# Kernel optimization log

Hardware: AMD Instinct MI355X
Metric: run time of the kernel (lower is better)

The kernel has to match this reference:

```python
import jax, jax.numpy as jnp
import numpy as np
import math

B, N, D, H, F = 2, 2048, 512, 8, 2048
DH = D // H
LN_EPS = 1e-5
PHASE_ALPHA = 0.1


def _layernorm(x, g, b):
    mu = jnp.mean(x, axis=-1, keepdims=True)
    var = jnp.mean(jnp.square(x - mu), axis=-1, keepdims=True)
    return (x - mu) * jax.lax.rsqrt(var + LN_EPS) * g + b


def setup_inputs() -> dict:
    key = jax.random.key(0)
    ks = jax.random.split(key, 16)
    s = 0.02
    return {
        "h": jax.random.normal(ks[0], (B, N, D), dtype=jnp.float32),
        "phases": jax.random.normal(ks[1], (B, N, H), dtype=jnp.float32),
        "mask": jnp.zeros((B, N), dtype=bool),
        "Wq": jax.random.normal(ks[2], (D, D), dtype=jnp.float32) * s,
        "Wk": jax.random.normal(ks[3], (D, D), dtype=jnp.float32) * s,
        "Wp": jax.random.normal(ks[4], (D, H), dtype=jnp.float32) * s,
        "bp": jnp.zeros((H,), dtype=jnp.float32),
        "Wv": jax.random.normal(ks[5], (D, D), dtype=jnp.float32) * s,
        "Wo": jax.random.normal(ks[6], (D, D), dtype=jnp.float32) * s,
        "W1": jax.random.normal(ks[7], (D, F), dtype=jnp.float32) * s,
        "b1": jnp.zeros((F,), dtype=jnp.float32),
        "W2": jax.random.normal(ks[8], (F, D), dtype=jnp.float32) * s,
        "b2": jnp.zeros((D,), dtype=jnp.float32),
        "g1": jnp.ones((D,), dtype=jnp.float32),
        "be1": jnp.zeros((D,), dtype=jnp.float32),
        "g2": jnp.ones((D,), dtype=jnp.float32),
        "be2": jnp.zeros((D,), dtype=jnp.float32),
        "Wph": jax.random.normal(ks[9], (D, H), dtype=jnp.float32) * s,
        "bph": jnp.zeros((H,), dtype=jnp.float32),
    }


def reference(h, phases, mask, Wq, Wk, Wp, bp, Wv, Wo, W1, b1, W2, b2, g1, be1, g2, be2, Wph, bph):
    # --- HarmonicEdgeLayer ---
    Q = (h @ Wq).reshape(B, N, H, DH)  # (B,N,H,dh)
    K = (h @ Wk).reshape(B, N, H, DH)
    scores = jnp.einsum("bnhd,bmhd->bhnm", Q, K) / math.sqrt(DH)  # (B,H,N,N)
    ph = h @ Wp + bp                       # (B,N,H)
    phi = jnp.transpose(ph, (0, 2, 1))     # (B,H,N)
    harmonic = jnp.cos(phi[:, :, :, None] - phi[:, :, None, :])  # (B,H,N,N)
    scores = scores * (1.0 + harmonic) * 0.5
    scores = jnp.where(mask[:, None, None, :], -jnp.inf, scores)
    edge_weights = jax.nn.softmax(scores, axis=-1)  # (B,H,N,N)

    # --- HarmonicNodeUpdate ---
    V = (h @ Wv).reshape(B, N, H, DH)
    messages = jnp.einsum("bhnm,bmhd->bnhd", edge_weights, V).reshape(B, N, D)
    messages = messages @ Wo
    h1 = _layernorm(h + messages, g1, be1)
    ffn = jax.nn.gelu(h1 @ W1 + b1, approximate=False) @ W2 + b2
    h2 = _layernorm(h1 + ffn, g2, be2)

    # --- PhaseUpdate ---
    phases_new = phases + PHASE_ALPHA * jnp.tanh(h2 @ Wph + bph) * math.pi

    # convergence metric
    delta = jnp.mean(jnp.linalg.norm(h2 - h, axis=-1))
    return h2, phases_new, delta
```

## Files before the change

kernel.cpp:

```cpp
#include <hip/hip_runtime.h>
#include <math.h>

#define BB 2
#define NN 2048
#define DD 512
#define HH 8
#define DHH 64
#define FF 2048
#define MROWS (BB*NN)
#define LN_EPS 1e-5f
#define PHASE_ALPHA 0.1f
#define PI_F 3.14159265358979323846f
#define SCALE 0.125f
#define QLD (3*DD)
#define LOG2E 1.44269504088896340736f

typedef __attribute__((ext_vector_type(8))) short  bf16x8;
typedef __attribute__((ext_vector_type(4))) float  f32x4;
typedef __attribute__((ext_vector_type(4))) unsigned short us4;

__device__ __forceinline__ unsigned short f2bf(float x) {
    unsigned int u = __float_as_uint(x);
    u += 0x7fffu + ((u >> 16) & 1u);
    return (unsigned short)(u >> 16);
}

#if __has_builtin(__builtin_amdgcn_exp2f)
#define EXP2(x) __builtin_amdgcn_exp2f(x)
#else
#define EXP2(x) exp2f(x)
#endif

__device__ __forceinline__ unsigned pk_bf16(float a, float b) {
    unsigned r;
    asm("v_cvt_pk_bf16_f32 %0, %1, %2" : "=v"(r) : "v"(a), "v"(b));
    return r;
}

__global__ __launch_bounds__(256) void convert_bf16_kernel(
    const float* __restrict__ X, unsigned short* __restrict__ Y, int n8)
{
    int i = blockIdx.x*256 + threadIdx.x;
    if (i >= n8) return;
    const float4 a = *(const float4*)&X[i*8];
    const float4 b = *(const float4*)&X[i*8 + 4];
    uint4 o;
    o.x = (unsigned)f2bf(a.x) | ((unsigned)f2bf(a.y) << 16);
    o.y = (unsigned)f2bf(a.z) | ((unsigned)f2bf(a.w) << 16);
    o.z = (unsigned)f2bf(b.x) | ((unsigned)f2bf(b.y) << 16);
    o.w = (unsigned)f2bf(b.z) | ((unsigned)f2bf(b.w) << 16);
    *(uint4*)&Y[i*8] = o;
}

__global__ __launch_bounds__(256) void wtrans_kernel(
    const float* __restrict__ W, unsigned short* __restrict__ WT, int K, int N)
{
    __shared__ unsigned short T[32][33];
    const int k0 = blockIdx.y*32, n0 = blockIdx.x*32;
    const int r = threadIdx.x >> 3, cc = (threadIdx.x & 7)*4;
    float4 v = *(const float4*)&W[(size_t)(k0 + r)*N + n0 + cc];
    T[cc+0][r] = f2bf(v.x); T[cc+1][r] = f2bf(v.y);
    T[cc+2][r] = f2bf(v.z); T[cc+3][r] = f2bf(v.w);
    __syncthreads();
    us4 o; o.x = T[r][cc]; o.y = T[r][cc+1]; o.z = T[r][cc+2]; o.w = T[r][cc+3];
    *(us4*)&WT[(size_t)(n0 + r)*K + k0 + cc] = o;
}

__global__ __launch_bounds__(256) void vtrans_kernel(
    const unsigned short* __restrict__ qkv, unsigned short* __restrict__ VT)
{
    __shared__ unsigned short T[32][33];
    const int b = blockIdx.z;
    const int n0 = blockIdx.x*32, c0 = blockIdx.y*32;
    const int r = threadIdx.x >> 3, cc = (threadIdx.x & 7)*4;
    us4 v = *(const us4*)&qkv[((size_t)b*NN + n0 + r)*QLD + 2*DD + c0 + cc];
    T[cc+0][r] = v.x; T[cc+1][r] = v.y; T[cc+2][r] = v.z; T[cc+3][r] = v.w;
    __syncthreads();
    const int cg = c0 + r;
    const int hh = cg >> 6, dh = cg & 63;
    us4 o; o.x = T[r][cc]; o.y = T[r][cc+1]; o.z = T[r][cc+2]; o.w = T[r][cc+3];
    *(us4*)&VT[(((size_t)b*HH + hh)*DHH + dh)*NN + n0 + cc] = o;
}

template<int BM, int BN, int SPLITK, int OUTBF16, int BIAS, int ACT, int ATOMIC>
__global__ __launch_bounds__(256, 2) void mfma_gemm(
    const unsigned short* __restrict__ A, const unsigned short* __restrict__ BT,
    const float* __restrict__ bias, void* __restrict__ Cout,
    int M, int Nc, int K)
{
    constexpr int FM = BM/32, FN = BN/32;
    constexpr int ROWS = BM + BN;
    constexpr int NLOAD = ROWS*8/256;
    __shared__ unsigned short Ss[ROWS][72];

    const int tid = threadIdx.x;
    const int w = tid >> 6, lane = tid & 63;
    const int c = lane & 15, g = lane >> 4;
    const int wr = w >> 1, wc = w & 1;
    const int bm = blockIdx.y*BM, bn = blockIdx.x*BN;
    const int k0 = (SPLITK > 1) ? blockIdx.z * (K / SPLITK) : 0;
    const int NT = (K / SPLITK) / 64;

    f32x4 zero = {0.f, 0.f, 0.f, 0.f};
    f32x4 acc[FM][FN];
    #pragma unroll
    for (int i = 0; i < FM; ++i)
        #pragma unroll
        for (int j = 0; j < FN; ++j) acc[i][j] = zero;

    uint4 pf[NLOAD];
    #pragma unroll
    for (int l = 0; l < NLOAD; ++l) {
        const int i = tid + l*256;
        const int r = i >> 3, kc = (i & 7)*8;
        const unsigned short* src = (r < BM) ? &A [(size_t)(bm + r)*K + k0 + kc]
                                             : &BT[(size_t)(bn + r - BM)*K + k0 + kc];
        pf[l] = *(const uint4*)src;
    }

    for (int kt = 0; kt < NT; ++kt) {
        __syncthreads();
        #pragma unroll
        for (int l = 0; l < NLOAD; ++l) {
            const int i = tid + l*256;
            *(uint4*)&Ss[i >> 3][(i & 7)*8] = pf[l];
        }
        __syncthreads();
        if (kt + 1 < NT) {
            #pragma unroll
            for (int l = 0; l < NLOAD; ++l) {
                const int i = tid + l*256;
                const int r = i >> 3, kc = (i & 7)*8;
                const unsigned short* src = (r < BM)
                    ? &A [(size_t)(bm + r)*K + k0 + (kt+1)*64 + kc]
                    : &BT[(size_t)(bn + r - BM)*K + k0 + (kt+1)*64 + kc];
                pf[l] = *(const uint4*)src;
            }
        }
        #pragma unroll
        for (int ks = 0; ks < 2; ++ks) {
            bf16x8 af[FM], bfr[FN];
            #pragma unroll
            for (int mf = 0; mf < FM; ++mf)
                af[mf] = *(const bf16x8*)&Ss[wr*(BM/2) + mf*16 + c][ks*32 + g*8];
            #pragma unroll
            for (int nf = 0; nf < FN; ++nf)
                bfr[nf] = *(const bf16x8*)&Ss[BM + wc*(BN/2) + nf*16 + c][ks*32 + g*8];
            #pragma unroll
            for (int mf = 0; mf < FM; ++mf)
                #pragma unroll
                for (int nf = 0; nf < FN; ++nf)
                    acc[mf][nf] = __builtin_amdgcn_mfma_f32_16x16x32_bf16(
                        af[mf], bfr[nf], acc[mf][nf], 0, 0, 0);
        }
    }

    #pragma unroll
    for (int mf = 0; mf < FM; ++mf)
        #pragma unroll
        for (int nf = 0; nf < FN; ++nf) {
            const int col = bn + wc*(BN/2) + nf*16 + c;
            const float bv = BIAS ? bias[col] : 0.f;
            #pragma unroll
            for (int r = 0; r < 4; ++r) {
                const int row = bm + wr*(BM/2) + mf*16 + g*4 + r;
                float x = acc[mf][nf][r] + bv;
                if (ACT == 1) x = 0.5f * x * (1.f + erff(x * 0.70710678118654752f));
                if (ATOMIC)       atomicAdd(&((float*)Cout)[(size_t)row*Nc + col], x);
                else if (OUTBF16) ((unsigned short*)Cout)[(size_t)row*Nc + col] = f2bf(x);
                else              ((float*)Cout)[(size_t)row*Nc + col] = x;
            }
        }
}

__global__ __launch_bounds__(256) void phase_proj_kernel(
    const float* __restrict__ X, const float* __restrict__ Wp,
    const float* __restrict__ bp, float* __restrict__ cosPt, float* __restrict__ sinPt)
{
    __shared__ float Wl[DD*HH];
    for (int i = threadIdx.x; i < DD*HH; i += 256) Wl[i] = Wp[i];
    __syncthreads();
    int row = blockIdx.x*32 + (threadIdx.x >> 3);
    int hh  = threadIdx.x & 7;
    const float* xr = X + (size_t)row * DD;
    float acc = bp[hh];
    for (int k = 0; k < DD; k += 4) {
        float4 xv = *(const float4*)&xr[k];
        acc += xv.x*Wl[(k  )*HH+hh] + xv.y*Wl[(k+1)*HH+hh]
             + xv.z*Wl[(k+2)*HH+hh] + xv.w*Wl[(k+3)*HH+hh];
    }
    const int b = row >> 11, n = row & (NN-1);
    cosPt[((size_t)b*HH + hh)*NN + n] = cosf(acc);
    sinPt[((size_t)b*HH + hh)*NN + n] = sinf(acc);
}

__global__ __launch_bounds__(256) void phase_update_kernel(
    const float* __restrict__ H2, const float* __restrict__ Wph,
    const float* __restrict__ bph, const float* __restrict__ phases,
    float* __restrict__ phases_out)
{
    __shared__ float Wl[DD*HH];
    for (int i = threadIdx.x; i < DD*HH; i += 256) Wl[i] = Wph[i];
    __syncthreads();
    int row = blockIdx.x*32 + (threadIdx.x >> 3);
    int hh  = threadIdx.x & 7;
    const float* xr = H2 + (size_t)row * DD;
    float acc = bph[hh];
    for (int k = 0; k < DD; k += 4) {
        float4 xv = *(const float4*)&xr[k];
        acc += xv.x*Wl[(k  )*HH+hh] + xv.y*Wl[(k+1)*HH+hh]
             + xv.z*Wl[(k+2)*HH+hh] + xv.w*Wl[(k+3)*HH+hh];
    }
    phases_out[row*HH + hh] = phases[row*HH + hh] + PHASE_ALPHA * tanhf(acc) * PI_F;
}

__global__ __launch_bounds__(256, 4) void attn_kernel(
    const unsigned short* __restrict__ qkv, const unsigned short* __restrict__ VT,
    const float* __restrict__ cosPt, const float* __restrict__ sinPt,
    const unsigned char* __restrict__ mask, unsigned short* __restrict__ msgb)
{
    __shared__ float Os[64][36];
    __shared__ float MwS[4][32], LwS[4][32];
    __shared__ unsigned short Pl[4][32][40];

    const int tid = threadIdx.x;
    const int w = tid >> 6, lane = tid & 63;
    const int c = lane & 15, g = lane >> 4;
    const int qBase = blockIdx.x * 32;
    const int hh = blockIdx.y, b = blockIdx.z;
    const size_t rowOff = (size_t)b * NN;
    const int bh = b*HH + hh;
    const size_t cosBase = (size_t)bh * NN;
    const float A = 0.5f * SCALE * LOG2E;

    for (int i = tid; i < 64*36; i += 256) ((float*)Os)[i] = 0.f;

    bf16x8 qf[2][2];
    #pragma unroll
    for (int nf = 0; nf < 2; ++nf)
        #pragma unroll
        for (int ks = 0; ks < 2; ++ks)
            qf[nf][ks] = *(const bf16x8*)&qkv[(rowOff + qBase + nf*16 + c)*QLD
                                              + hh*DHH + ks*32 + g*8];
    float cqs[2], sqs[2];
    #pragma unroll
    for (int nf = 0; nf < 2; ++nf) {
        cqs[nf] = A * cosPt[cosBase + qBase + nf*16 + c];
        sqs[nf] = A * sinPt[cosBase + qBase + nf*16 + c];
    }

    f32x4 zero = {0.f, 0.f, 0.f, 0.f};
    f32x4 acc[4][2];
    #pragma unroll
    for (int i = 0; i < 4; ++i)
        #pragma unroll
        for (int j = 0; j < 2; ++j) acc[i][j] = zero;
    float mst[2] = {-INFINITY, -INFINITY}, lst[2] = {0.f, 0.f};

    __syncthreads();

    for (int s = w; s < NN/32; s += 4) {
        const int kb0 = s * 32;
        f32x4 st[2][2];
        #pragma unroll
        for (int mf = 0; mf < 2; ++mf) {
            bf16x8 kf0 = *(const bf16x8*)&qkv[(rowOff + kb0 + mf*16 + c)*QLD + DD + hh*DHH + g*8];
            bf16x8 kf1 = *(const bf16x8*)&qkv[(rowOff + kb0 + mf*16 + c)*QLD + DD + hh*DHH + 32 + g*8];
            #pragma unroll
            for (int nf = 0; nf < 2; ++nf) {
                st[mf][nf] = __builtin_amdgcn_mfma_f32_16x16x32_bf16(kf0, qf[nf][0], zero, 0, 0, 0);
                st[mf][nf] = __builtin_amdgcn_mfma_f32_16x16x32_bf16(kf1, qf[nf][1], st[mf][nf], 0, 0, 0);
            }
        }
        #pragma unroll
        for (int mf = 0; mf < 2; ++mf) {
            const int keyb = kb0 + mf*16 + g*4;
            const f32x4 ck = *(const f32x4*)&cosPt[cosBase + keyb];
            const f32x4 sk = *(const f32x4*)&sinPt[cosBase + keyb];
            const unsigned int mk = *(const unsigned int*)&mask[rowOff + keyb];
            f32x4 mbias;
            #pragma unroll
            for (int r = 0; r < 4; ++r)
                mbias[r] = ((mk >> (8*r)) & 0xff) ? -INFINITY : 0.f;
            #pragma unroll
            for (int nf = 0; nf < 2; ++nf)
                #pragma unroll
                for (int r = 0; r < 4; ++r) {
                    const float factor = fmaf(cqs[nf], ck[r], fmaf(sqs[nf], sk[r], A));
                    st[mf][nf][r] = fmaf(st[mf][nf][r], factor, mbias[r]);
                }
        }
        #pragma unroll
        for (int nf = 0; nf < 2; ++nf) {
            float tmax = fmaxf(fmaxf(st[0][nf][0], st[0][nf][1]), fmaxf(st[0][nf][2], st[0][nf][3]));
            tmax = fmaxf(tmax, fmaxf(fmaxf(st[1][nf][0], st[1][nf][1]), fmaxf(st[1][nf][2], st[1][nf][3])));
            tmax = fmaxf(tmax, __shfl_xor(tmax, 16));
            tmax = fmaxf(tmax, __shfl_xor(tmax, 32));
            if (!__all(tmax <= mst[nf])) {
                const float mnew = fmaxf(mst[nf], tmax);
                const float corr = (mst[nf] == -INFINITY) ? 0.f : EXP2(mst[nf] - mnew);
                lst[nf] *= corr;
                #pragma unroll
                for (int mo = 0; mo < 4; ++mo)
                    #pragma unroll
                    for (int r = 0; r < 4; ++r) acc[mo][nf][r] *= corr;
                mst[nf] = mnew;
            }
            const float mcur = mst[nf];
            float psum = 0.f;
            unsigned short* prow = &Pl[w][nf*16 + c][0];
            #pragma unroll
            for (int mf = 0; mf < 2; ++mf) {
                float p0 = EXP2(st[mf][nf][0] - mcur);
                float p1 = EXP2(st[mf][nf][1] - mcur);
                float p2 = EXP2(st[mf][nf][2] - mcur);
                float p3 = EXP2(st[mf][nf][3] - mcur);
                psum += (p0 + p1) + (p2 + p3);
                uint2 pk; pk.x = pk_bf16(p0, p1); pk.y = pk_bf16(p2, p3);
                *(uint2*)&prow[mf*16 + g*4] = pk;
            }
            psum += __shfl_xor(psum, 16);
            psum += __shfl_xor(psum, 32);
            lst[nf] += psum;
        }
        bf16x8 vf[4], pfr[2];
        #pragma unroll
        for (int mo = 0; mo < 4; ++mo)
            vf[mo] = *(const bf16x8*)&VT[((size_t)bh*DHH + mo*16 + c)*NN + kb0 + g*8];
        #pragma unroll
        for (int nf = 0; nf < 2; ++nf)
            pfr[nf] = *(const bf16x8*)&Pl[w][nf*16 + c][g*8];
        #pragma unroll
        for (int mo = 0; mo < 4; ++mo)
            #pragma unroll
            for (int nf = 0; nf < 2; ++nf)
                acc[mo][nf] = __builtin_amdgcn_mfma_f32_16x16x32_bf16(
                    vf[mo], pfr[nf], acc[mo][nf], 0, 0, 0);
    }

    if (lane < 16) {
        #pragma unroll
        for (int nf = 0; nf < 2; ++nf) {
            MwS[w][nf*16 + lane] = mst[nf];
            LwS[w][nf*16 + lane] = lst[nf];
        }
    }
    __syncthreads();
    float fac[2];
    #pragma unroll
    for (int nf = 0; nf < 2; ++nf) {
        const int q = nf*16 + c;
        float M = fmaxf(fmaxf(MwS[0][q], MwS[1][q]), fmaxf(MwS[2][q], MwS[3][q]));
        float L = LwS[0][q]*EXP2(MwS[0][q]-M) + LwS[1][q]*EXP2(MwS[1][q]-M)
                + LwS[2][q]*EXP2(MwS[2][q]-M) + LwS[3][q]*EXP2(MwS[3][q]-M);
        fac[nf] = EXP2(mst[nf] - M) / L;
    }
    #pragma unroll
    for (int mo = 0; mo < 4; ++mo)
        #pragma unroll
        for (int nf = 0; nf < 2; ++nf)
            #pragma unroll
            for (int r = 0; r < 4; ++r)
                atomicAdd(&Os[mo*16 + g*4 + r][nf*16 + c], acc[mo][nf][r] * fac[nf]);
    __syncthreads();

    const int q = tid >> 3, dh0 = (tid & 7) * 8;
    unsigned int ov[4];
    #pragma unroll
    for (int i = 0; i < 4; ++i)
        ov[i] = (unsigned)f2bf(Os[dh0 + 2*i][q]) | ((unsigned)f2bf(Os[dh0 + 2*i + 1][q]) << 16);
    unsigned short* op = &msgb[(rowOff + qBase + q)*DD + hh*DHH + dh0];
    *(uint4*)&op[0] = *(uint4*)&ov[0];
}

template<int WITH_DELTA, int WBF16, int YBIAS>
__global__ __launch_bounds__(256) void ln_kernel(
    const float* __restrict__ x, const float* __restrict__ y,
    const float* __restrict__ g, const float* __restrict__ bvec,
    const float* __restrict__ ybias,
    float* __restrict__ out, unsigned short* __restrict__ outb,
    const float* __restrict__ href, float* __restrict__ deltaAcc)
{
    const int row = blockIdx.x;
    const int tid = threadIdx.x;
    const size_t base = (size_t)row * DD + tid*2;
    float2 xv = *(const float2*)(x + base);
    float2 yv = *(const float2*)(y + base);
    float v0 = xv.x + yv.x;
    float v1 = xv.y + yv.y;
    if (YBIAS) { v0 += ybias[tid*2]; v1 += ybias[tid*2+1]; }
    float s  = v0 + v1;
    float sq = v0*v0 + v1*v1;
    #pragma unroll
    for (int m = 1; m < 64; m <<= 1) {
        s  += __shfl_xor(s,  m, 64);
        sq += __shfl_xor(sq, m, 64);
    }
    __shared__ float redS[4], redQ[4];
    int wv = tid >> 6;
    if ((tid & 63) == 0) { redS[wv] = s; redQ[wv] = sq; }
    __syncthreads();
    s  = redS[0] + redS[1] + redS[2] + redS[3];
    sq = redQ[0] + redQ[1] + redQ[2] + redQ[3];
    float mu  = s * (1.f/DD);
    float var = sq * (1.f/DD) - mu*mu;
    float inv = rsqrtf(var + LN_EPS);
    float o0 = (v0 - mu)*inv*g[tid*2  ] + bvec[tid*2  ];
    float o1 = (v1 - mu)*inv*g[tid*2+1] + bvec[tid*2+1];
    float2 ov; ov.x = o0; ov.y = o1;
    *(float2*)(out + base) = ov;
    if (WBF16)
        ((unsigned int*)outb)[(size_t)row*(DD/2) + tid] =
            (unsigned)f2bf(o0) | ((unsigned)f2bf(o1) << 16);

    if (WITH_DELTA) {
        float d0 = o0 - href[base], d1 = o1 - href[base + 1];
        float ds = d0*d0 + d1*d1;
        #pragma unroll
        for (int m = 1; m < 64; m <<= 1) ds += __shfl_xor(ds, m, 64);
        __shared__ float redD[4];
        if ((tid & 63) == 0) redD[wv] = ds;
        __syncthreads();
        if (tid == 0) {
            float t = redD[0] + redD[1] + redD[2] + redD[3];
            atomicAdd(deltaAcc, sqrtf(t));
        }
    }
}

__global__ void delta_finalize(const float* __restrict__ acc, float* __restrict__ out)
{
    out[0] = acc[0] * (1.f / (float)MROWS);
}

extern "C" void kernel_launch(void* const* d_in, const int* in_sizes, int n_in,
                              void* d_out, int out_size, void* d_ws, size_t ws_size,
                              hipStream_t stream)
{
    (void)in_sizes; (void)n_in; (void)out_size; (void)ws_size;
    const float* h      = (const float*)d_in[0];
    const float* phases = (const float*)d_in[1];
    const unsigned char* mask = (const unsigned char*)d_in[2];
    const float* Wq  = (const float*)d_in[3];
    const float* Wk  = (const float*)d_in[4];
    const float* Wp  = (const float*)d_in[5];
    const float* bp  = (const float*)d_in[6];
    const float* Wv  = (const float*)d_in[7];
    const float* Wo  = (const float*)d_in[8];
    const float* W1  = (const float*)d_in[9];
    const float* b1  = (const float*)d_in[10];
    const float* W2  = (const float*)d_in[11];
    const float* b2  = (const float*)d_in[12];
    const float* g1  = (const float*)d_in[13];
    const float* be1 = (const float*)d_in[14];
    const float* g2  = (const float*)d_in[15];
    const float* be2 = (const float*)d_in[16];
    const float* Wph = (const float*)d_in[17];
    const float* bph = (const float*)d_in[18];

    char* ws = (char*)d_ws;
    const size_t MB = 1024*1024;
    unsigned short* hb   = (unsigned short*)(ws);
    unsigned short* WqT  = (unsigned short*)(ws + 4*MB);
    unsigned short* WkT  = (unsigned short*)(ws + 4*MB + 512*1024);
    unsigned short* WvT  = (unsigned short*)(ws + 5*MB);
    unsigned short* WoT  = (unsigned short*)(ws + 5*MB + 512*1024);
    unsigned short* W1T  = (unsigned short*)(ws + 6*MB);
    unsigned short* W2T  = (unsigned short*)(ws + 8*MB);
    unsigned short* qkvb = (unsigned short*)(ws + 10*MB);
    unsigned short* VT   = (unsigned short*)(ws + 22*MB);
    unsigned short* T1b  = qkvb;
    unsigned short* msgb = (unsigned short*)(ws + 26*MB);
    float* mo    = (float*)(ws + 30*MB);
    float* ffn   = mo;
    float* h1    = (float*)(ws + 38*MB);
    unsigned short* h1b = (unsigned short*)(ws + 46*MB);
    float* cosPt = (float*)(ws + 50*MB);
    float* sinPt = (float*)(ws + 50*MB + 64*1024);
    float* dAcc  = (float*)(ws + 50*MB + 128*1024);

    float* out_h2    = (float*)d_out;
    float* out_ph    = out_h2 + (size_t)MROWS*DD;
    float* out_delta = out_ph + MROWS*HH;

    hipMemsetAsync(dAcc, 0, sizeof(float), stream);

    dim3 blk(256);
    convert_bf16_kernel<<<dim3(MROWS*DD/8/256), blk, 0, stream>>>(h, hb, MROWS*DD/8);
    wtrans_kernel<<<dim3(DD/32, DD/32), blk, 0, stream>>>(Wq, WqT, DD, DD);
    wtrans_kernel<<<dim3(DD/32, DD/32), blk, 0, stream>>>(Wk, WkT, DD, DD);
    wtrans_kernel<<<dim3(DD/32, DD/32), blk, 0, stream>>>(Wv, WvT, DD, DD);
    wtrans_kernel<<<dim3(DD/32, DD/32), blk, 0, stream>>>(Wo, WoT, DD, DD);
    wtrans_kernel<<<dim3(FF/32, DD/32), blk, 0, stream>>>(W1, W1T, DD, FF);
    wtrans_kernel<<<dim3(DD/32, FF/32), blk, 0, stream>>>(W2, W2T, FF, DD);
    phase_proj_kernel<<<dim3(MROWS/32), blk, 0, stream>>>(h, Wp, bp, cosPt, sinPt);
    mfma_gemm<64,128,1,1,0,0,0><<<dim3((3*DD)/128, MROWS/64), blk, 0, stream>>>(
        hb, WqT, nullptr, qkvb, MROWS, 3*DD, DD);
    vtrans_kernel<<<dim3(NN/32, DD/32, BB), blk, 0, stream>>>(qkvb, VT);
    attn_kernel<<<dim3(NN/32, HH, BB), blk, 0, stream>>>(qkvb, VT, cosPt, sinPt, mask, msgb);
    mfma_gemm<64,64,1,0,0,0,0><<<dim3(DD/64, MROWS/64), blk, 0, stream>>>(
        msgb, WoT, nullptr, mo, MROWS, DD, DD);
    ln_kernel<0,1,0><<<dim3(MROWS), blk, 0, stream>>>(h, mo, g1, be1, nullptr, h1, h1b, nullptr, nullptr);
    mfma_gemm<128,128,1,1,1,1,0><<<dim3(FF/128, MROWS/128), blk, 0, stream>>>(
        h1b, W1T, b1, T1b, MROWS, FF, DD);
    hipMemsetAsync(ffn, 0, (size_t)MROWS*DD*sizeof(float), stream);
    mfma_gemm<64,64,2,0,0,0,1><<<dim3(DD/64, MROWS/64, 2), blk, 0, stream>>>(
        T1b, W2T, nullptr, ffn, MROWS, DD, FF);
    ln_kernel<1,0,1><<<dim3(MROWS), blk, 0, stream>>>(h1, ffn, g2, be2, b2, out_h2, nullptr, h, dAcc);
    phase_update_kernel<<<dim3(MROWS/32), blk, 0, stream>>>(out_h2, Wph, bph, phases, out_ph);
    delta_finalize<<<dim3(1), dim3(1), 0, stream>>>(dAcc, out_delta);
}
```

Baseline: 523.7 us.

## Double query tile per attention block and prefetch next K tile

Each attention block now handles 64 queries instead of 32, so every K and V fragment loaded from global memory feeds twice as many MFMAs. K fragments for the next key tile are loaded into registers while the current tile is processed, and the V load is hoisted ahead of the score MFMAs. s_setprio raises wave priority around the MFMA bursts. This doubles the accumulator and score register footprint (launch bounds drop to 2 blocks per CU) and halves the grid to 512 blocks, which lowers occupancy.

```diff
diff --git a/kernel.cpp b/kernel.cpp
--- a/kernel.cpp
+++ b/kernel.cpp
@@ -214,64 +214,91 @@
     phases_out[row*HH + hh] = phases[row*HH + hh] + PHASE_ALPHA * tanhf(acc) * PI_F;
 }
 
-__global__ __launch_bounds__(256, 4) void attn_kernel(
+__global__ __launch_bounds__(256, 2) void attn_kernel(
     const unsigned short* __restrict__ qkv, const unsigned short* __restrict__ VT,
     const float* __restrict__ cosPt, const float* __restrict__ sinPt,
     const unsigned char* __restrict__ mask, unsigned short* __restrict__ msgb)
 {
-    __shared__ float Os[64][36];
-    __shared__ float MwS[4][32], LwS[4][32];
-    __shared__ unsigned short Pl[4][32][40];
+    __shared__ float Os[64][68];
+    __shared__ float MwS[4][64], LwS[4][64];
+    __shared__ unsigned short Pl[4][64][40];
 
     const int tid = threadIdx.x;
     const int w = tid >> 6, lane = tid & 63;
     const int c = lane & 15, g = lane >> 4;
-    const int qBase = blockIdx.x * 32;
+    const int qBase = blockIdx.x * 64;
     const int hh = blockIdx.y, b = blockIdx.z;
     const size_t rowOff = (size_t)b * NN;
     const int bh = b*HH + hh;
     const size_t cosBase = (size_t)bh * NN;
     const float A = 0.5f * SCALE * LOG2E;
 
-    for (int i = tid; i < 64*36; i += 256) ((float*)Os)[i] = 0.f;
-
-    bf16x8 qf[2][2];
-    #pragma unroll
-    for (int nf = 0; nf < 2; ++nf)
+    for (int i = tid; i < 64*68; i += 256) ((float*)Os)[i] = 0.f;
+
+    bf16x8 qf[4][2];
+    #pragma unroll
+    for (int nf = 0; nf < 4; ++nf)
         #pragma unroll
         for (int ks = 0; ks < 2; ++ks)
             qf[nf][ks] = *(const bf16x8*)&qkv[(rowOff + qBase + nf*16 + c)*QLD
                                               + hh*DHH + ks*32 + g*8];
-    float cqs[2], sqs[2];
-    #pragma unroll
-    for (int nf = 0; nf < 2; ++nf) {
+    float cqs[4], sqs[4];
+    #pragma unroll
+    for (int nf = 0; nf < 4; ++nf) {
         cqs[nf] = A * cosPt[cosBase + qBase + nf*16 + c];
         sqs[nf] = A * sinPt[cosBase + qBase + nf*16 + c];
     }
 
     f32x4 zero = {0.f, 0.f, 0.f, 0.f};
-    f32x4 acc[4][2];
+    f32x4 acc[4][4];
     #pragma unroll
     for (int i = 0; i < 4; ++i)
         #pragma unroll
-        for (int j = 0; j < 2; ++j) acc[i][j] = zero;
-    float mst[2] = {-INFINITY, -INFINITY}, lst[2] = {0.f, 0.f};
+        for (int j = 0; j < 4; ++j) acc[i][j] = zero;
+    float mst[4] = {-INFINITY, -INFINITY, -INFINITY, -INFINITY};
+    float lst[4] = {0.f, 0.f, 0.f, 0.f};
+
+    const unsigned short* kbase = &qkv[rowOff*QLD + DD + hh*DHH];
+    bf16x8 kcur[2][2], knxt[2][2];
+    {
+        const int kb0 = w * 32;
+        #pragma unroll
+        for (int mf = 0; mf < 2; ++mf)
+            #pragma unroll
+            for (int ks = 0; ks < 2; ++ks)
+                kcur[mf][ks] = *(const bf16x8*)&kbase[(size_t)(kb0 + mf*16 + c)*QLD + ks*32 + g*8];
+    }
 
     __syncthreads();
 
     for (int s = w; s < NN/32; s += 4) {
         const int kb0 = s * 32;
-        f32x4 st[2][2];
-        #pragma unroll
-        for (int mf = 0; mf < 2; ++mf) {
-            bf16x8 kf0 = *(const bf16x8*)&qkv[(rowOff + kb0 + mf*16 + c)*QLD + DD + hh*DHH + g*8];
-            bf16x8 kf1 = *(const bf16x8*)&qkv[(rowOff + kb0 + mf*16 + c)*QLD + DD + hh*DHH + 32 + g*8];
-            #pragma unroll
-            for (int nf = 0; nf < 2; ++nf) {
-                st[mf][nf] = __builtin_amdgcn_mfma_f32_16x16x32_bf16(kf0, qf[nf][0], zero, 0, 0, 0);
-                st[mf][nf] = __builtin_amdgcn_mfma_f32_16x16x32_bf16(kf1, qf[nf][1], st[mf][nf], 0, 0, 0);
+        bf16x8 vf[4];
+        #pragma unroll
+        for (int mo = 0; mo < 4; ++mo)
+            vf[mo] = *(const bf16x8*)&VT[((size_t)bh*DHH + mo*16 + c)*NN + kb0 + g*8];
+
+        f32x4 st[2][4];
+        __builtin_amdgcn_s_setprio(1);
+        #pragma unroll
+        for (int mf = 0; mf < 2; ++mf)
+            #pragma unroll
+            for (int nf = 0; nf < 4; ++nf) {
+                st[mf][nf] = __builtin_amdgcn_mfma_f32_16x16x32_bf16(kcur[mf][0], qf[nf][0], zero, 0, 0, 0);
+                st[mf][nf] = __builtin_amdgcn_mfma_f32_16x16x32_bf16(kcur[mf][1], qf[nf][1], st[mf][nf], 0, 0, 0);
             }
-        }
+        __builtin_amdgcn_s_setprio(0);
+
+        {
+            const int sn = (s + 4 < NN/32) ? s + 4 : s;
+            const int kn0 = sn * 32;
+            #pragma unroll
+            for (int mf = 0; mf < 2; ++mf)
+                #pragma unroll
+                for (int ks = 0; ks < 2; ++ks)
+                    knxt[mf][ks] = *(const bf16x8*)&kbase[(size_t)(kn0 + mf*16 + c)*QLD + ks*32 + g*8];
+        }
+
         #pragma unroll
         for (int mf = 0; mf < 2; ++mf) {
             const int keyb = kb0 + mf*16 + g*4;
@@ -283,15 +310,16 @@
             for (int r = 0; r < 4; ++r)
                 mbias[r] = ((mk >> (8*r)) & 0xff) ? -INFINITY : 0.f;
             #pragma unroll
-            for (int nf = 0; nf < 2; ++nf)
+            for (int nf = 0; nf < 4; ++nf)
                 #pragma unroll
                 for (int r = 0; r < 4; ++r) {
                     const float factor = fmaf(cqs[nf], ck[r], fmaf(sqs[nf], sk[r], A));
                     st[mf][nf][r] = fmaf(st[mf][nf][r], factor, mbias[r]);
                 }
         }
-        #pragma unroll
-        for (int nf = 0; nf < 2; ++nf) {
+
+        #pragma unroll
+        for (int nf = 0; nf < 4; ++nf) {
             float tmax = fmaxf(fmaxf(st[0][nf][0], st[0][nf][1]), fmaxf(st[0][nf][2], st[0][nf][3]));
             tmax = fmaxf(tmax, fmaxf(fmaxf(st[1][nf][0], st[1][nf][1]), fmaxf(st[1][nf][2], st[1][nf][3])));
             tmax = fmaxf(tmax, __shfl_xor(tmax, 16));
@@ -323,32 +351,38 @@
             psum += __shfl_xor(psum, 32);
             lst[nf] += psum;
         }
-        bf16x8 vf[4], pfr[2];
+
+        bf16x8 pfr[4];
+        #pragma unroll
+        for (int nf = 0; nf < 4; ++nf)
+            pfr[nf] = *(const bf16x8*)&Pl[w][nf*16 + c][g*8];
+        __builtin_amdgcn_s_setprio(1);
         #pragma unroll
         for (int mo = 0; mo < 4; ++mo)
-            vf[mo] = *(const bf16x8*)&VT[((size_t)bh*DHH + mo*16 + c)*NN + kb0 + g*8];
-        #pragma unroll
-        for (int nf = 0; nf < 2; ++nf)
-            pfr[nf] = *(const bf16x8*)&Pl[w][nf*16 + c][g*8];
-        #pragma unroll
-        for (int mo = 0; mo < 4; ++mo)
-            #pragma unroll
-            for (int nf = 0; nf < 2; ++nf)
+            #pragma unroll
+            for (int nf = 0; nf < 4; ++nf)
                 acc[mo][nf] = __builtin_amdgcn_mfma_f32_16x16x32_bf16(
                     vf[mo], pfr[nf], acc[mo][nf], 0, 0, 0);
+        __builtin_amdgcn_s_setprio(0);
+
+        #pragma unroll
+        for (int mf = 0; mf < 2; ++mf)
+            #pragma unroll
+            for (int ks = 0; ks < 2; ++ks)
+                kcur[mf][ks] = knxt[mf][ks];
     }
 
     if (lane < 16) {
         #pragma unroll
-        for (int nf = 0; nf < 2; ++nf) {
+        for (int nf = 0; nf < 4; ++nf) {
             MwS[w][nf*16 + lane] = mst[nf];
             LwS[w][nf*16 + lane] = lst[nf];
         }
     }
     __syncthreads();
-    float fac[2];
-    #pragma unroll
-    for (int nf = 0; nf < 2; ++nf) {
+    float fac[4];
+    #pragma unroll
+    for (int nf = 0; nf < 4; ++nf) {
         const int q = nf*16 + c;
         float M = fmaxf(fmaxf(MwS[0][q], MwS[1][q]), fmaxf(MwS[2][q], MwS[3][q]));
         float L = LwS[0][q]*EXP2(MwS[0][q]-M) + LwS[1][q]*EXP2(MwS[1][q]-M)
@@ -358,19 +392,20 @@
     #pragma unroll
     for (int mo = 0; mo < 4; ++mo)
         #pragma unroll
-        for (int nf = 0; nf < 2; ++nf)
+        for (int nf = 0; nf < 4; ++nf)
             #pragma unroll
             for (int r = 0; r < 4; ++r)
                 atomicAdd(&Os[mo*16 + g*4 + r][nf*16 + c], acc[mo][nf][r] * fac[nf]);
     __syncthreads();
 
-    const int q = tid >> 3, dh0 = (tid & 7) * 8;
-    unsigned int ov[4];
-    #pragma unroll
-    for (int i = 0; i < 4; ++i)
+    const int q = tid >> 2, dh0 = (tid & 3) * 16;
+    unsigned int ov[8];
+    #pragma unroll
+    for (int i = 0; i < 8; ++i)
         ov[i] = (unsigned)f2bf(Os[dh0 + 2*i][q]) | ((unsigned)f2bf(Os[dh0 + 2*i + 1][q]) << 16);
     unsigned short* op = &msgb[(rowOff + qBase + q)*DD + hh*DHH + dh0];
     *(uint4*)&op[0] = *(uint4*)&ov[0];
+    *(uint4*)&op[8] = *(uint4*)&ov[4];
 }
 
 template<int WITH_DELTA, int WBF16, int YBIAS>
@@ -497,7 +532,7 @@
     mfma_gemm<64,128,1,1,0,0,0><<<dim3((3*DD)/128, MROWS/64), blk, 0, stream>>>(
         hb, WqT, nullptr, qkvb, MROWS, 3*DD, DD);
     vtrans_kernel<<<dim3(NN/32, DD/32, BB), blk, 0, stream>>>(qkvb, VT);
-    attn_kernel<<<dim3(NN/32, HH, BB), blk, 0, stream>>>(qkvb, VT, cosPt, sinPt, mask, msgb);
+    attn_kernel<<<dim3(NN/64, HH, BB), blk, 0, stream>>>(qkvb, VT, cosPt, sinPt, mask, msgb);
     mfma_gemm<64,64,1,0,0,0,0><<<dim3(DD/64, MROWS/64), blk, 0, stream>>>(
         msgb, WoT, nullptr, mo, MROWS, DD, DD);
     ln_kernel<0,1,0><<<dim3(MROWS), blk, 0, stream>>>(h, mo, g1, be1, nullptr, h1, h1b, nullptr, nullptr);
```

Measured after the change: 493.4 us. -5.8%, faster.
